# Optimization experiments

Hardware: AMD Instinct MI355X
Metric: run time of the kernel (lower is better)

The kernel has to match this reference:

```python
import jax, jax.numpy as jnp
import numpy as np
from jax import lax

DN = ('NCHW', 'OIHW', 'NCHW')
NUM_CODES = 8192


def _conv(x, w, b):
    # Conv2d(k=4, s=2, p=1)
    y = lax.conv_general_dilated(x, w, (2, 2), ((1, 1), (1, 1)), dimension_numbers=DN)
    return y + b[None, :, None, None]


def _convT(x, w, b):
    # ConvTranspose2d(k=4, s=2, p=1) as lhs-dilated conv; kernel already in equivalent OIHW layout
    y = lax.conv_general_dilated(x, w, (1, 1), ((2, 2), (2, 2)), lhs_dilation=(2, 2), dimension_numbers=DN)
    return y + b[None, :, None, None]


def _aff(x, s, b):
    # eval-mode BatchNorm folded to per-channel affine
    return x * s[None, :, None, None] + b[None, :, None, None]


def _forward(x, ew1, eb1, bn1s, bn1b, ew2, eb2, bn2s, bn2b, ew3, eb3, bn3s, bn3b, ew4, eb4, embed, cluster_size, dw1, db1, dbn1s, dbn1b, dw2, db2, dbn2s, dbn2b, dw3, db3, dbn3s, dbn3b, dw4, db4):
    sg = lax.stop_gradient
    embed = sg(embed)          # codebook is a torch buffer -> no grad
    cluster_size = sg(cluster_size)
    relu = jax.nn.relu
    # ---- Encoder: 4 stride-2 convs ----
    h = relu(_aff(_conv(x, ew1, eb1), bn1s, bn1b))
    h = relu(_aff(_conv(h, ew2, eb2), bn2s, bn2b))
    h = relu(_aff(_conv(h, ew3, eb3), bn3s, bn3b))
    z = _conv(h, ew4, eb4)                       # [B, D, G, G]
    zt = jnp.transpose(z, (0, 2, 3, 1))          # [B, G, G, D]
    D = zt.shape[-1]
    flat = zt.reshape(-1, D)                     # [N, D]
    N = flat.shape[0]
    # ---- VQ: pairwise squared distance + argmin codebook lookup ----
    dist = (flat * flat).sum(1, keepdims=True) - 2.0 * (flat @ embed.T) + (embed * embed).sum(1)[None, :]
    soft = jax.nn.softmax(-dist, axis=-1)        # temperature = 1.0
    codes = jnp.argmin(dist, axis=1)             # [N]
    zq = embed[codes]                            # [N, D]
    commitment_loss = jnp.mean((flat - sg(zq)) ** 2)
    codebook_loss = jnp.mean((zq - sg(flat)) ** 2)
    avg_soft = soft.mean(0)
    usage_entropy = -(avg_soft * jnp.log(avg_soft + 1e-10)).sum()
    diversity_loss = -usage_entropy / float(np.log(NUM_CODES))
    zq_st = flat + sg(zq - flat)                 # straight-through estimator
    zq_grid = jnp.transpose(zq_st.reshape(zt.shape), (0, 3, 1, 2))  # [B, D, G, G]
    # ---- Decoder: 4 stride-2 transposed convs ----
    h = relu(_aff(_convT(zq_grid, dw1, db1), dbn1s, dbn1b))
    h = relu(_aff(_convT(h, dw2, db2), dbn2s, dbn2b))
    h = relu(_aff(_convT(h, dw3, db3), dbn3s, dbn3b))
    recon = jax.nn.sigmoid(_convT(h, dw4, db4))
    recon_loss = jnp.mean((recon - x) ** 2)
    # ---- usage stats (no-grad in torch) ----
    hard_avg = jnp.zeros(NUM_CODES, flat.dtype).at[codes].add(1.0) / N
    perplexity = jnp.exp(-(hard_avg * jnp.log(hard_avg + 1e-10)).sum())
    active_codes = (cluster_size > 1).sum()
    codes_grid = codes.reshape(zt.shape[:-1])
    return (recon, recon_loss, codes_grid, zq_grid, commitment_loss, codebook_loss, diversity_loss, usage_entropy, perplexity, active_codes)


def setup_inputs() -> dict:
    keys = iter(jax.random.split(jax.random.key(0), 64))
    def randn(shape, s=1.0):
        return jax.random.normal(next(keys), shape, jnp.float32) * s
    def randu(shape):
        return jax.random.uniform(next(keys), shape, dtype=jnp.float32)
    B, H = 32, 256
    return {
        'x': randu((B, 1, H, H)),
        'ew1': randn((64, 1, 4, 4), 0.25), 'eb1': randn((64,), 0.1),
        'bn1s': randu((64,)), 'bn1b': randn((64,), 0.1),
        'ew2': randn((64, 64, 4, 4), 0.03), 'eb2': randn((64,), 0.1),
        'bn2s': randu((64,)), 'bn2b': randn((64,), 0.1),
        'ew3': randn((128, 64, 4, 4), 0.03), 'eb3': randn((128,), 0.1),
        'bn3s': randu((128,)), 'bn3b': randn((128,), 0.1),
        'ew4': randn((64, 128, 4, 4), 0.02), 'eb4': randn((64,), 0.1),
        'embed': randn((8192, 64), 0.5),
        'cluster_size': jnp.ones((8192,), jnp.float32),
        'dw1': randn((128, 64, 4, 4), 0.03), 'db1': randn((128,), 0.1),
        'dbn1s': randu((128,)), 'dbn1b': randn((128,), 0.1),
        'dw2': randn((64, 128, 4, 4), 0.02), 'db2': randn((64,), 0.1),
        'dbn2s': randu((64,)), 'dbn2b': randn((64,), 0.1),
        'dw3': randn((64, 64, 4, 4), 0.03), 'db3': randn((64,), 0.1),
        'dbn3s': randu((64,)), 'dbn3b': randn((64,), 0.1),
        'dw4': randn((1, 64, 4, 4), 0.03), 'db4': randn((1,), 0.1),
    }


def reference(x, ew1, eb1, bn1s, bn1b, ew2, eb2, bn2s, bn2b, ew3, eb3, bn3s, bn3b, ew4, eb4, embed, cluster_size, dw1, db1, dbn1s, dbn1b, dw2, db2, dbn2s, dbn2b, dw3, db3, dbn3s, dbn3b, dw4, db4):
    return _forward(x, ew1, eb1, bn1s, bn1b, ew2, eb2, bn2s, bn2b, ew3, eb3, bn3s, bn3b, ew4, eb4, embed, cluster_size, dw1, db1, dbn1s, dbn1b, dw2, db2, dbn2s, dbn2b, dw3, db3, dbn3s, dbn3b, dw4, db4)
```

## Files before the change

kernel.cpp:

```cpp
#include <hip/hip_runtime.h>
#include <cstdint>
#include <cstddef>


#define DEVI __device__ __forceinline__

typedef short  short8 __attribute__((ext_vector_type(8)));
typedef __bf16 bf16x8 __attribute__((ext_vector_type(8)));
typedef float  f32x16 __attribute__((ext_vector_type(16)));

DEVI f32x16 MFMA(bf16x8 a, bf16x8 b, f32x16 c){
  return __builtin_amdgcn_mfma_f32_32x32x16_bf16(a, b, c, 0, 0, 0);
}

DEVI ushort f2bf(float f){
  unsigned u = __float_as_uint(f);
  unsigned r = (u + 0x7FFFu + ((u >> 16) & 1u)) >> 16;
  return (ushort)r;
}
DEVI float bf2f(ushort h){ return __uint_as_float(((unsigned)h) << 16); }

union U8 { short8 s; bf16x8 b; };
DEVI bf16x8 ldg8u(const ushort* p){
  U8 u; u.s = *(const short8*)p; return u.b;
}

DEVI float wred64(float v){
  #pragma unroll
  for (int off=32; off>0; off>>=1) v += __shfl_down(v, off, 64);
  return v;
}

#define O_RECON     0
#define O_RLOSS     2097152
#define O_CODES     2097153
#define O_ZQ        2105345
#define O_COMMIT    2629633
#define O_CB        2629634
#define O_DIV       2629635
#define O_UE        2629636
#define O_PERP      2629637
#define O_ACT       2629638

#define WS_R1       0ull
#define A3H_OFF     0ull
#define A3M_OFF     8912896ull
#define A3L_OFF     17825792ull
#define PP_OFF      33554432ull
#define MT_OFF      37748736ull
#define PARTA_OFF   41943040ull
#define A2H_OFF     134217728ull
#define A2M_OFF     151519232ull
#define A2L_OFF     168820736ull
#define EH_OFF      134217728ull
#define EM_OFF      135266304ull
#define EL_OFF      136314880ull
#define FH_OFF      137363456ull
#define FM_OFF      138412032ull
#define FL_OFF      139460608ull
#define D2H_OFF     134217728ull
#define D2L_OFF     151519232ull
#define D1H_OFF     168820736ull
#define D1L_OFF     177733632ull
#define WS_FLAT     186646528ull
#define WS_ZQP      188743680ull
#define WS_WT       191102976ull
#define WT_E2       (WS_WT)
#define WT_E3       (WT_E2 + 393216ull)
#define WT_E4       (WT_E3 + 786432ull)
#define WT_D1       (WT_E4 + 786432ull)
#define WT_D2       (WT_D1 + 524288ull)
#define WT_D3       (WT_D2 + 524288ull)
#define WS_W4       (WT_D3 + 262144ull)
#define WS_STATS    (WS_W4 + 4096ull)
#define ST_RMP      (WS_STATS)
#define ST_CNT      (ST_RMP + 65536ull)
#define ST_AVGS     (ST_CNT + 32768ull)
#define ST_ROWZI    (ST_AVGS + 32768ull)
#define ST_CODESQ   (ST_ROWZI + 32768ull)
#define ST_LOSS     (ST_CODESQ + 32768ull)

__global__ __launch_bounds__(256) void k_init(unsigned int* __restrict__ cnt,
                                              unsigned long long* __restrict__ rmp,
                                              float* __restrict__ loss)
{
  int i = blockIdx.x*256 + threadIdx.x;
  if (i < 8192){ cnt[i]=0u; rmp[i]=0xFFFFFFFFFFFFFFFFull; }
  if (i < 8) loss[i]=0.f;
}

__global__ __launch_bounds__(256) void k_wsplit(
    const float* __restrict__ src, ushort* __restrict__ dh,
    ushort* __restrict__ dm, ushort* __restrict__ dl,
    int OC, int CIN, int isT, int three)
{
  int i = blockIdx.x*256 + threadIdx.x;
  if (i >= 16*OC*CIN) return;
  int cin = i % CIN; int t = i / CIN; int oc = t % OC; int tap = t / OC;
  int st;
  if (isT){
    int pq = tap>>2, ab = tap&3;
    int p = pq>>1, q = pq&1, a = ab>>1, b = ab&1;
    st = (p + 2*a)*4 + (q + 2*b);
  } else st = tap;
  float v = src[((size_t)oc*CIN + cin)*16 + st];
  ushort h = f2bf(v); float r = v - bf2f(h);
  if (three){
    ushort m = f2bf(r); float r2 = r - bf2f(m);
    dm[i] = m; dl[i] = f2bf(r2);
  } else {
    dl[i] = f2bf(r);
  }
  dh[i] = h;
}

__global__ __launch_bounds__(256) void k_w4prep(const float* __restrict__ dw4,
                                                float* __restrict__ w4)
{
  int i = blockIdx.x*256 + threadIdx.x;
  if (i >= 1024) return;
  int c = i & 63; int t16 = i >> 6;
  int pq = t16 >> 2, ab = t16 & 3;
  int p = pq>>1, q = pq&1, a = ab>>1, b = ab&1;
  w4[i] = dw4[(size_t)c*16 + (p+2*a)*4 + (q+2*b)];
}

__global__ __launch_bounds__(256) void k_esplit(
    const float* __restrict__ src, ushort* __restrict__ dh,
    ushort* __restrict__ dm, ushort* __restrict__ dl)
{
  int i = blockIdx.x*256 + threadIdx.x;
  float v = src[i];
  ushort h = f2bf(v); float r1 = v - bf2f(h);
  ushort m = f2bf(r1); float r2 = r1 - bf2f(m);
  dh[i] = h; dm[i] = m; dl[i] = f2bf(r2);
}

__global__ __launch_bounds__(256) void k_zpad3(unsigned* __restrict__ b0,
                                               unsigned* __restrict__ b1,
                                               unsigned* __restrict__ b2,
                                               int rows, int Wp, int cwords)
{
  int i = blockIdx.x*256 + threadIdx.x;
  int total = rows*2*cwords;
  if (i >= total) return;
  int pos = i / cwords, cw = i % cwords;
  int row = pos >> 1, side = pos & 1;
  size_t w = ((size_t)row*Wp + (side ? (Wp-1) : 0))*cwords + cw;
  b0[w] = 0u;
  if (b1) b1[w] = 0u;
  if (b2) b2[w] = 0u;
}

__global__ __launch_bounds__(256) void enc_conv1(
    const float* __restrict__ x, const float* __restrict__ w,
    const float* __restrict__ cb_, const float* __restrict__ bns,
    const float* __restrict__ bnb, float* __restrict__ out)
{
  __shared__ __align__(16) float sIn[34][36];
  __shared__ __align__(16) float sW[64][16];
  int b = blockIdx.x;
  int t = b & 63, n = b >> 6;
  int ty = t >> 3, tx = t & 7;
  int oy0 = ty*16, ox0 = tx*16;
  int iy0 = 2*oy0 - 1, ix0 = 2*ox0 - 1;
  int tid = threadIdx.x;
  int spg = tid & 31, og = tid >> 5;
  int sy = spg >> 1, x0 = (spg & 1)*8;

  if (tid < 64){
    const float* wp = w + tid*16;
    *(float4*)&sW[tid][0]  = *(const float4*)(wp);
    *(float4*)&sW[tid][4]  = *(const float4*)(wp+4);
    *(float4*)&sW[tid][8]  = *(const float4*)(wp+8);
    *(float4*)&sW[tid][12] = *(const float4*)(wp+12);
  }
  for (int e = tid; e < 34*34; e += 256){
    int rr = e/34, cc = e%34;
    int iy = iy0+rr, ix = ix0+cc;
    float v = 0.f;
    if ((unsigned)iy < 256u && (unsigned)ix < 256u)
      v = x[(size_t)n*65536 + iy*256 + ix];
    sIn[rr][cc] = v;
  }
  __syncthreads();

  float acc[8][8];
  #pragma unroll
  for (int j=0;j<8;j++)
    #pragma unroll
    for (int xi=0;xi<8;xi++) acc[j][xi]=0.f;

  #pragma unroll
  for (int ky=0; ky<4; ky++){
    int riy = 2*sy + ky;
    float seg[20];
    #pragma unroll
    for (int i=0;i<5;i++){
      float4 v = *(const float4*)&sIn[riy][2*x0 + 4*i];
      seg[4*i+0]=v.x; seg[4*i+1]=v.y; seg[4*i+2]=v.z; seg[4*i+3]=v.w;
    }
    #pragma unroll
    for (int j=0;j<8;j++){
      float4 w4v = *(const float4*)&sW[og*8+j][ky*4];
      #pragma unroll
      for (int xi=0; xi<8; xi++){
        acc[j][xi] = fmaf(seg[2*xi+0], w4v.x,
                     fmaf(seg[2*xi+1], w4v.y,
                     fmaf(seg[2*xi+2], w4v.z,
                     fmaf(seg[2*xi+3], w4v.w, acc[j][xi]))));
      }
    }
  }

  float sc[8], sh[8];
  #pragma unroll
  for (int j=0;j<8;j++){
    int oc = og*8+j;
    sc[j] = bns[oc];
    sh[j] = fmaf(cb_[oc], sc[j], bnb[oc]);
  }
  int oy = oy0 + sy;
  #pragma unroll
  for (int xi=0; xi<8; xi++){
    int oxg = ox0 + x0 + xi;
    float* op = out + (((size_t)n*128 + oy)*128 + oxg)*64 + og*8;
    float4 q0, q1;
    q0.x = fmaxf(fmaf(acc[0][xi], sc[0], sh[0]), 0.f);
    q0.y = fmaxf(fmaf(acc[1][xi], sc[1], sh[1]), 0.f);
    q0.z = fmaxf(fmaf(acc[2][xi], sc[2], sh[2]), 0.f);
    q0.w = fmaxf(fmaf(acc[3][xi], sc[3], sh[3]), 0.f);
    q1.x = fmaxf(fmaf(acc[4][xi], sc[4], sh[4]), 0.f);
    q1.y = fmaxf(fmaf(acc[5][xi], sc[5], sh[5]), 0.f);
    q1.z = fmaxf(fmaf(acc[6][xi], sc[6], sh[6]), 0.f);
    q1.w = fmaxf(fmaf(acc[7][xi], sc[7], sh[7]), 0.f);
    *(float4*)op     = q0;
    *(float4*)(op+4) = q1;
  }
}

template<int CIN, int OC, int OUTW, int OUTH, int INW, int INH, bool XPAD,
         int INMODE, int OUTMODE>
__global__ __launch_bounds__(256) void enc_conv(
    const float* __restrict__ in,
    const ushort* __restrict__ aH, const ushort* __restrict__ aM,
    const ushort* __restrict__ aL,
    const ushort* __restrict__ wtH, const ushort* __restrict__ wtM,
    const ushort* __restrict__ wtL,
    const float* __restrict__ cb_, const float* __restrict__ bns,
    const float* __restrict__ bnb,
    float* __restrict__ outF,
    ushort* __restrict__ oH, ushort* __restrict__ oM, ushort* __restrict__ oL,
    int nOcg)
{
  constexpr int INWP  = (INMODE==1) ? (INW+2) : (XPAD ? (INW+2) : INW);
  constexpr int WP    = INW + 2;
  constexpr int NROWS = 64 / OUTW;
  constexpr int AELEM = NROWS * WP * CIN;
  constexpr int BCIN  = (CIN > 64) ? 64 : CIN;
  constexpr int BELEM = 64 * BCIN;
  constexpr int SCRSZ = (3*BELEM*2 > 64*68*4) ? 3*BELEM*2 : 64*68*4;

  __shared__ __align__(16) ushort sAh[AELEM], sAm[AELEM], sAl[AELEM];
  __shared__ __align__(16) char sScr[SCRSZ];
  ushort* sBh = (ushort*)sScr;
  ushort* sBm = sBh + BELEM;
  ushort* sBl = sBm + BELEM;
  float*  sC  = (float*)sScr;

  int b = blockIdx.x;
  int ocg = b % nOcg; b /= nOcg;
  int yb  = b % (OUTH/NROWS); b /= (OUTH/NROWS);
  int n = b;
  int oy0 = yb * NROWS, oc0 = ocg * 64;

  int tid = threadIdx.x;
  int l = tid & 63, wave = tid >> 6;
  int wm = wave >> 1, wn = wave & 1;
  int r = l & 31, kp = l >> 5;
  int idx = wm*32 + r;
  int oy_off = idx / OUTW, ox = idx % OUTW;

  f32x16 acc;
  #pragma unroll
  for (int i=0;i<16;i++) acc[i] = 0.f;

  const size_t nbase = (size_t)n * INH * INWP * CIN;

  for (int ky = 0; ky < 4; ky++){
    __syncthreads();
    for (int c = tid; c < AELEM/8; c += 256){
      int j  = c / (WP*CIN/8);
      int rm = c % (WP*CIN/8);
      int lx = rm / (CIN/8);
      int c8 = (rm % (CIN/8)) * 8;
      int iy = 2*(oy0 + j) - 1 + ky;
      bool ok = (unsigned)iy < (unsigned)INH;
      unsigned off = (unsigned)(((j*WP + lx)*CIN + c8)*2) ^ ((((unsigned)lx>>1)&7u)<<4);
      if constexpr (INMODE == 0){
        int gx = XPAD ? lx : (lx - 1);
        if (!XPAD) ok = ok && ((unsigned)gx < (unsigned)INW);
        float4 v0 = {0,0,0,0}, v1 = {0,0,0,0};
        if (ok){
          const float* s = in + nbase + ((size_t)iy*INWP + gx)*CIN + c8;
          v0 = *(const float4*)s; v1 = *(const float4*)(s+4);
        }
        float vv[8] = {v0.x,v0.y,v0.z,v0.w,v1.x,v1.y,v1.z,v1.w};
        short8 hh, mm, ll;
        #pragma unroll
        for (int e=0;e<8;e++){
          ushort h = f2bf(vv[e]); float r1 = vv[e] - bf2f(h);
          ushort m = f2bf(r1);    float r2 = r1 - bf2f(m);
          hh[e] = (short)h; mm[e] = (short)m; ll[e] = (short)f2bf(r2);
        }
        *(short8*)((char*)sAh + off) = hh;
        *(short8*)((char*)sAm + off) = mm;
        *(short8*)((char*)sAl + off) = ll;
      } else {
        short8 vh = {0,0,0,0,0,0,0,0}, vm = vh, vl = vh;
        if (ok){
          size_t s = nbase + ((size_t)iy*INWP + lx)*CIN + c8;
          vh = *(const short8*)(aH + s);
          vm = *(const short8*)(aM + s);
          vl = *(const short8*)(aL + s);
        }
        *(short8*)((char*)sAh + off) = vh;
        *(short8*)((char*)sAm + off) = vm;
        *(short8*)((char*)sAl + off) = vl;
      }
    }
    for (int kx = 0; kx < 4; kx++){
      int tap = ky*4 + kx;
      for (int ch = 0; ch < CIN; ch += BCIN){
        __syncthreads();
        for (int c = tid; c < BELEM/8; c += 256){
          int oc = c / (BCIN/8);
          int c8 = (c % (BCIN/8)) * 8;
          size_t s = ((size_t)tap*OC + oc0 + oc)*CIN + ch + c8;
          unsigned off = (unsigned)((oc*BCIN + c8)*2) ^ (((unsigned)oc&7u)<<4);
          *(short8*)((char*)sBh + off) = *(const short8*)(wtH + s);
          *(short8*)((char*)sBm + off) = *(const short8*)(wtM + s);
          *(short8*)((char*)sBl + off) = *(const short8*)(wtL + s);
        }
        __syncthreads();
        int lx = 2*ox + kx;
        unsigned asw  = ((((unsigned)lx>>1)&7u)<<4);
        unsigned alin = (unsigned)(((oy_off*WP + lx)*CIN)*2);
        int ocl = wn*32 + r;
        unsigned bsw  = (((unsigned)ocl&7u)<<4);
        unsigned blin = (unsigned)((ocl*BCIN)*2);
        #pragma unroll
        for (int ct = 0; ct < BCIN/16; ct++){
          unsigned kbA = (unsigned)((ch + ct*16 + kp*8)*2);
          unsigned kbB = (unsigned)((ct*16 + kp*8)*2);
          unsigned ao = (alin + kbA) ^ asw;
          unsigned bo = (blin + kbB) ^ bsw;
          bf16x8 ah = *(const bf16x8*)((char*)sAh + ao);
          bf16x8 am = *(const bf16x8*)((char*)sAm + ao);
          bf16x8 al = *(const bf16x8*)((char*)sAl + ao);
          bf16x8 bh = *(const bf16x8*)((char*)sBh + bo);
          bf16x8 bm = *(const bf16x8*)((char*)sBm + bo);
          bf16x8 bl = *(const bf16x8*)((char*)sBl + bo);
          acc = MFMA(ah, bh, acc);
          acc = MFMA(ah, bm, acc);
          acc = MFMA(am, bh, acc);
          acc = MFMA(ah, bl, acc);
          acc = MFMA(am, bm, acc);
          acc = MFMA(al, bh, acc);
        }
      }
    }
  }
  __syncthreads();
  #pragma unroll
  for (int q = 0; q < 16; q++){
    int rowt = (q&3) + 8*(q>>2) + 4*kp;
    sC[(wm*32 + rowt)*68 + wn*32 + r] = acc[q];
  }
  __syncthreads();
  {
    int m = tid >> 2, qq = tid & 3;
    int oc = oc0 + qq*16;
    int oyg = oy0 + m / OUTW;
    int oxg = m % OUTW;
    if constexpr (OUTMODE == 1){
      size_t row = (size_t)n*256 + oyg*16 + oxg;
      float* op = outF + row*64 + qq*16;
      size_t pb = row*64 + qq*16;
      short8 hv[2], mv[2], lv[2];
      #pragma unroll
      for (int i=0;i<16;i++){
        float v = sC[m*68 + qq*16 + i] + cb_[oc+i];
        op[i] = v;
        ushort h = f2bf(v); float r1 = v - bf2f(h);
        ushort mm = f2bf(r1); float r2 = r1 - bf2f(mm);
        hv[i>>3][i&7]=(short)h; mv[i>>3][i&7]=(short)mm; lv[i>>3][i&7]=(short)f2bf(r2);
      }
      *(short8*)(oH + pb) = hv[0]; *(short8*)(oH + pb + 8) = hv[1];
      *(short8*)(oM + pb) = mv[0]; *(short8*)(oM + pb + 8) = mv[1];
      *(short8*)(oL + pb) = lv[0]; *(short8*)(oL + pb + 8) = lv[1];
    } else {
      size_t pbase = (((size_t)n*OUTH + oyg)*(OUTW+2) + oxg + 1)*OC + oc;
      short8 hv[2], mv[2], lv[2];
      #pragma unroll
      for (int i=0;i<16;i++){
        float s1 = bns[oc+i];
        float s2 = fmaf(cb_[oc+i], s1, bnb[oc+i]);
        float v = fmaxf(fmaf(sC[m*68 + qq*16 + i], s1, s2), 0.f);
        ushort h = f2bf(v); float r1 = v - bf2f(h);
        ushort mm = f2bf(r1); float r2 = r1 - bf2f(mm);
        hv[i>>3][i&7]=(short)h; mv[i>>3][i&7]=(short)mm; lv[i>>3][i&7]=(short)f2bf(r2);
      }
      *(short8*)(oH + pbase)   = hv[0]; *(short8*)(oH + pbase+8) = hv[1];
      *(short8*)(oM + pbase)   = mv[0]; *(short8*)(oM + pbase+8) = mv[1];
      *(short8*)(oL + pbase)   = lv[0]; *(short8*)(oL + pbase+8) = lv[1];
    }
  }
}

__global__ __launch_bounds__(256) void k_codesq(const float* __restrict__ embed,
                                                float* __restrict__ codesq)
{
  int j = blockIdx.x*4 + (threadIdx.x>>6);
  int c = threadIdx.x & 63;
  float e = embed[(size_t)j*64 + c];
  float s = wred64(e*e);
  if (c==0) codesq[j] = s;
}

DEVI float rmp_minval(unsigned long long v){
  unsigned skey = (unsigned)(v >> 32);
  unsigned u = (skey & 0x80000000u) ? (skey ^ 0x80000000u) : ~skey;
  return __uint_as_float(u);
}

__global__ __launch_bounds__(256) void vq_min(
    const ushort* __restrict__ fH, const ushort* __restrict__ fM,
    const ushort* __restrict__ fL,
    const ushort* __restrict__ eH, const ushort* __restrict__ eM,
    const ushort* __restrict__ eL,
    const float* __restrict__ codesq,
    unsigned long long* __restrict__ rmp,
    float* __restrict__ Pp, float* __restrict__ Mt)
{
  __shared__ __align__(16) ushort sAh[128*64], sAm[128*64], sAl[128*64];
  int cb = blockIdx.x & 63, rb = blockIdx.x >> 6;
  int row0 = rb*128, c0 = cb*128;
  int tid = threadIdx.x, l = tid&63, wave = tid>>6;
  int wm = wave>>1, wn = wave&1, r = l&31, kp = l>>5;

  for (int c = tid; c < 1024; c += 256){
    int rr = c >> 3, c8 = (c & 7)*8;
    size_t s = (size_t)(row0+rr)*64 + c8;
    unsigned off = (unsigned)((rr*64 + c8)*2) ^ (((unsigned)rr&7u)<<4);
    *(short8*)((char*)sAh + off) = *(const short8*)(fH + s);
    *(short8*)((char*)sAm + off) = *(const short8*)(fM + s);
    *(short8*)((char*)sAl + off) = *(const short8*)(fL + s);
  }
  __syncthreads();

  f32x16 acc[2][2];
  #pragma unroll
  for (int mt=0;mt<2;mt++)
    #pragma unroll
    for (int nt=0;nt<2;nt++)
      #pragma unroll
      for (int i=0;i<16;i++) acc[mt][nt][i]=0.f;

  #pragma unroll
  for (int ks=0; ks<4; ks++){
    unsigned kb = (unsigned)((ks*16 + kp*8)*2);
    int ko = ks*16 + kp*8;
    bf16x8 Ah[2],Am[2],Al[2],Bh[2],Bm[2],Bl[2];
    #pragma unroll
    for (int mt=0;mt<2;mt++){
      int rowi = wm*64 + mt*32 + r;
      unsigned o = ((unsigned)(rowi*128) + kb) ^ (((unsigned)rowi&7u)<<4);
      Ah[mt] = *(const bf16x8*)((char*)sAh + o);
      Am[mt] = *(const bf16x8*)((char*)sAm + o);
      Al[mt] = *(const bf16x8*)((char*)sAl + o);
    }
    #pragma unroll
    for (int nt=0;nt<2;nt++){
      int coli = c0 + wn*64 + nt*32 + r;
      size_t bo = (size_t)coli*64 + ko;
      Bh[nt] = ldg8u(eH + bo);
      Bm[nt] = ldg8u(eM + bo);
      Bl[nt] = ldg8u(eL + bo);
    }
    #pragma unroll
    for (int mt=0;mt<2;mt++)
      #pragma unroll
      for (int nt=0;nt<2;nt++){
        acc[mt][nt] = MFMA(Ah[mt], Bh[nt], acc[mt][nt]);
        acc[mt][nt] = MFMA(Ah[mt], Bm[nt], acc[mt][nt]);
        acc[mt][nt] = MFMA(Am[mt], Bh[nt], acc[mt][nt]);
        acc[mt][nt] = MFMA(Ah[mt], Bl[nt], acc[mt][nt]);
        acc[mt][nt] = MFMA(Am[mt], Bm[nt], acc[mt][nt]);
        acc[mt][nt] = MFMA(Al[mt], Bh[nt], acc[mt][nt]);
      }
  }

  float cq[2];
  cq[0] = codesq[c0 + wn*64 + r];
  cq[1] = codesq[c0 + wn*64 + 32 + r];
  #pragma unroll
  for (int mt=0; mt<2; mt++){
    #pragma unroll
    for (int q=0; q<16; q++){
      int rowt = (q&3) + 8*(q>>2) + 4*kp;
      int grow = row0 + wm*64 + mt*32 + rowt;
      float dv[2];
      unsigned long long kmin = 0xFFFFFFFFFFFFFFFFull;
      #pragma unroll
      for (int nt=0; nt<2; nt++){
        int col = c0 + wn*64 + nt*32 + r;
        float d = cq[nt] - 2.f*acc[mt][nt][q];
        dv[nt] = d;
        unsigned u = __float_as_uint(d);
        unsigned sgn = (unsigned)((int)u >> 31);
        unsigned skey = u ^ (sgn | 0x80000000u);
        unsigned long long key = (((unsigned long long)skey)<<32) | (unsigned)col;
        if (key < kmin) kmin = key;
      }
      #pragma unroll
      for (int off2=16; off2>0; off2>>=1){
        unsigned long long o2 = __shfl_xor(kmin, off2, 64);
        if (o2 < kmin) kmin = o2;
      }
      float mloc = rmp_minval(kmin);
      float p = __expf(mloc - dv[0]) + __expf(mloc - dv[1]);
      #pragma unroll
      for (int off2=16; off2>0; off2>>=1) p += __shfl_xor(p, off2, 64);
      if (r == 0){
        atomicMin(&rmp[grow], kmin);
        size_t pidx = (size_t)grow*128 + (size_t)cb*2 + wn;
        Pp[pidx] = p;
        Mt[pidx] = mloc;
      }
    }
  }
}

__global__ __launch_bounds__(256) void k_rowz2(
    const unsigned long long* __restrict__ rmp,
    const float* __restrict__ Pp, const float* __restrict__ Mt,
    float* __restrict__ rowzi)
{
  int row = blockIdx.x*256 + threadIdx.x;
  float mg = rmp_minval(rmp[row]);
  const float* pp = Pp + (size_t)row*128;
  const float* mt = Mt + (size_t)row*128;
  float z = 0.f;
  for (int t = 0; t < 128; t++)
    z = fmaf(__expf(mg - mt[t]), pp[t], z);
  rowzi[row] = 1.f / z;
}

__global__ __launch_bounds__(256) void vq_avg(
    const ushort* __restrict__ fH, const ushort* __restrict__ fM,
    const ushort* __restrict__ fL,
    const ushort* __restrict__ eH, const ushort* __restrict__ eM,
    const ushort* __restrict__ eL,
    const float* __restrict__ codesq,
    const unsigned long long* __restrict__ rmp,
    const float* __restrict__ rowzi,
    float* __restrict__ partA)
{
  __shared__ __align__(16) ushort sAh[128*64], sAm[128*64], sAl[128*64];
  __shared__ float colbuf[128];
  int cb = blockIdx.x & 63, rb = blockIdx.x >> 6;
  int row0 = rb*128, c0 = cb*128;
  int tid = threadIdx.x, l = tid&63, wave = tid>>6;
  int wm = wave>>1, wn = wave&1, r = l&31, kp = l>>5;

  if (tid < 128) colbuf[tid] = 0.f;

  for (int c = tid; c < 1024; c += 256){
    int rr = c >> 3, c8 = (c & 7)*8;
    size_t s = (size_t)(row0+rr)*64 + c8;
    unsigned off = (unsigned)((rr*64 + c8)*2) ^ (((unsigned)rr&7u)<<4);
    *(short8*)((char*)sAh + off) = *(const short8*)(fH + s);
    *(short8*)((char*)sAm + off) = *(const short8*)(fM + s);
    *(short8*)((char*)sAl + off) = *(const short8*)(fL + s);
  }
  __syncthreads();

  f32x16 acc[2][2];
  #pragma unroll
  for (int mt=0;mt<2;mt++)
    #pragma unroll
    for (int nt=0;nt<2;nt++)
      #pragma unroll
      for (int i=0;i<16;i++) acc[mt][nt][i]=0.f;

  #pragma unroll
  for (int ks=0; ks<4; ks++){
    unsigned kb = (unsigned)((ks*16 + kp*8)*2);
    int ko = ks*16 + kp*8;
    bf16x8 Ah[2],Am[2],Al[2],Bh[2],Bm[2],Bl[2];
    #pragma unroll
    for (int mt=0;mt<2;mt++){
      int rowi = wm*64 + mt*32 + r;
      unsigned o = ((unsigned)(rowi*128) + kb) ^ (((unsigned)rowi&7u)<<4);
      Ah[mt] = *(const bf16x8*)((char*)sAh + o);
      Am[mt] = *(const bf16x8*)((char*)sAm + o);
      Al[mt] = *(const bf16x8*)((char*)sAl + o);
    }
    #pragma unroll
    for (int nt=0;nt<2;nt++){
      int coli = c0 + wn*64 + nt*32 + r;
      size_t bo = (size_t)coli*64 + ko;
      Bh[nt] = ldg8u(eH + bo);
      Bm[nt] = ldg8u(eM + bo);
      Bl[nt] = ldg8u(eL + bo);
    }
    #pragma unroll
    for (int mt=0;mt<2;mt++)
      #pragma unroll
      for (int nt=0;nt<2;nt++){
        acc[mt][nt] = MFMA(Ah[mt], Bh[nt], acc[mt][nt]);
        acc[mt][nt] = MFMA(Ah[mt], Bm[nt], acc[mt][nt]);
        acc[mt][nt] = MFMA(Am[mt], Bh[nt], acc[mt][nt]);
        acc[mt][nt] = MFMA(Ah[mt], Bl[nt], acc[mt][nt]);
        acc[mt][nt] = MFMA(Am[mt], Bm[nt], acc[mt][nt]);
        acc[mt][nt] = MFMA(Al[mt], Bh[nt], acc[mt][nt]);
      }
  }

  float cq[2];
  cq[0] = codesq[c0 + wn*64 + r];
  cq[1] = codesq[c0 + wn*64 + 32 + r];
  float colacc[2] = {0.f, 0.f};
  #pragma unroll
  for (int mt=0; mt<2; mt++){
    #pragma unroll
    for (int q=0; q<16; q++){
      int rowt = (q&3) + 8*(q>>2) + 4*kp;
      int grow = row0 + wm*64 + mt*32 + rowt;
      float mi = rmp_minval(rmp[grow]);
      float zi = rowzi[grow];
      #pragma unroll
      for (int nt=0; nt<2; nt++){
        float d = cq[nt] - 2.f*acc[mt][nt][q];
        colacc[nt] = fmaf(__expf(mi - d), zi, colacc[nt]);
      }
    }
  }
  #pragma unroll
  for (int nt=0; nt<2; nt++){
    float o = __shfl_xor(colacc[nt], 32, 64);
    colacc[nt] += o;
    if (l < 32) atomicAdd(&colbuf[wn*64 + nt*32 + r], colacc[nt]);
  }
  __syncthreads();
  if (tid < 128)
    partA[(size_t)rb*8192 + c0 + tid] = colbuf[tid];
}

__global__ __launch_bounds__(256) void k_avgred(const float* __restrict__ partA,
                                                float* __restrict__ avgs)
{
  int j = blockIdx.x*256 + threadIdx.x;
  float s = 0.f;
  for (int rb = 0; rb < 64; rb++)
    s += partA[(size_t)rb*8192 + j];
  avgs[j] = s;
}

__global__ __launch_bounds__(256) void vq_post(
    const float* __restrict__ flat, const float* __restrict__ embed,
    const unsigned long long* __restrict__ rmp,
    float* __restrict__ out_codes, float* __restrict__ out_zq,
    ushort* __restrict__ zqPh, ushort* __restrict__ zqPl,
    float* __restrict__ loss, unsigned int* __restrict__ cnt)
{
  int r = blockIdx.x*4 + (threadIdx.x>>6);
  int c = threadIdx.x & 63;
  unsigned j = (unsigned)(rmp[r] & 0xFFFFFFFFull);
  float e = embed[(size_t)j*64 + c];
  float f = flat[(size_t)r*64 + c];
  int n = r>>8, rem = r&255, gy = rem>>4, gx = rem&15;
  out_zq[(((size_t)n*64 + c)*16 + gy)*16 + gx] = e;
  ushort h = f2bf(e);
  size_t pz = (((size_t)n*16 + gy)*18 + gx + 1)*64 + c;
  zqPh[pz] = h; zqPl[pz] = f2bf(e - bf2f(h));
  float d = f - e;
  float s2 = wred64(d*d);
  if (c==0){
    out_codes[r] = (float)j;
    atomicAdd(cnt + j, 1u);
    atomicAdd(loss + 1, s2);
  }
}

template<int CIN, int OC, int SW, int SH, bool OUTPAD, int OMODE, int NPAR>
__global__ __launch_bounds__(256) void dec_convT_m(
    const ushort* __restrict__ inH, const ushort* __restrict__ inL,
    const ushort* __restrict__ wtH, const ushort* __restrict__ wtL,
    const float* __restrict__ db, const float* __restrict__ bns,
    const float* __restrict__ bnb,
    ushort* __restrict__ oH, ushort* __restrict__ oL, int nOcg)
{
  constexpr int TR    = 64 / SW;
  constexpr int NRA   = TR + ((NPAR==4) ? 2 : 1);
  constexpr int WPin  = SW + 2;
  constexpr int AELEM = NRA * WPin * CIN;
  constexpr int OUTH  = 2*SH;
  constexpr int OW    = OUTPAD ? (2*SW+2) : (2*SW);

  __shared__ __align__(16) ushort sAh[AELEM], sAl[AELEM];
  __shared__ __align__(16) float sC[64*68];

  int b = blockIdx.x;
  int p_blk = 0;
  if (NPAR == 2){ p_blk = b & 1; b >>= 1; }
  int ocg = b % nOcg; b /= nOcg;
  int tb = b % (SH/TR); b /= (SH/TR);
  int n = b;
  int t0 = tb * TR, oc0 = ocg * 64;
  const int ROWBASE = (NPAR==4) ? -1 : (p_blk - 1);

  int tid = threadIdx.x, l = tid&63, wave = tid>>6;
  int wm = wave>>1, wn = wave&1;
  int r = l&31, kp = l>>5;
  int idx = wm*32 + r;
  int t_off = idx / SW, s = idx % SW;
  int ocl = oc0 + wn*32 + r;

  for (int c = tid; c < AELEM/8; c += 256){
    int j  = c / (WPin*CIN/8);
    int rm = c % (WPin*CIN/8);
    int lx = rm / (CIN/8);
    int c8 = (rm % (CIN/8)) * 8;
    int giy = t0 + ROWBASE + j;
    bool ok = (unsigned)giy < (unsigned)SH;
    short8 vh = {0,0,0,0,0,0,0,0}, vl = {0,0,0,0,0,0,0,0};
    if (ok){
      size_t sidx = (((size_t)n*SH + giy)*WPin + lx)*CIN + c8;
      vh = *(const short8*)(inH + sidx);
      vl = *(const short8*)(inL + sidx);
    }
    unsigned off = (unsigned)(((j*WPin + lx)*CIN + c8)*2) ^ (((unsigned)lx&7u)<<4);
    *(short8*)((char*)sAh + off) = vh;
    *(short8*)((char*)sAl + off) = vl;
  }
  __syncthreads();

  for (int pr = 0; pr < NPAR; pr++){
    int p2 = (NPAR==4) ? (pr>>1) : p_blk;
    int q2 = (NPAR==4) ? (pr&1)  : pr;
    int par = p2*2 + q2;

    f32x16 acc;
    #pragma unroll
    for (int i=0;i<16;i++) acc[i]=0.f;

    for (int ab = 0; ab < 4; ab++){
      int a = ab>>1, bb = ab&1;
      int rs = t_off + ((NPAR==4) ? (p2 + a) : a);
      int lx = s + q2 + bb;
      unsigned asw  = (((unsigned)lx&7u)<<4);
      unsigned alin = (unsigned)(((rs*WPin + lx)*CIN)*2);
      size_t brow = ((size_t)(par*4 + ab)*OC + ocl)*CIN;
      #pragma unroll
      for (int ct = 0; ct < CIN/16; ct++){
        int ko = ct*16 + kp*8;
        unsigned ao = (alin + (unsigned)(ko*2)) ^ asw;
        bf16x8 ah = *(const bf16x8*)((char*)sAh + ao);
        bf16x8 al = *(const bf16x8*)((char*)sAl + ao);
        bf16x8 bh = ldg8u(wtH + brow + ko);
        bf16x8 bl = ldg8u(wtL + brow + ko);
        acc = MFMA(ah, bh, acc);
        acc = MFMA(ah, bl, acc);
        acc = MFMA(al, bh, acc);
      }
    }

    __syncthreads();
    #pragma unroll
    for (int qre = 0; qre < 16; qre++){
      int rowt = (qre&3) + 8*(qre>>2) + 4*kp;
      sC[(wm*32 + rowt)*68 + wn*32 + r] = acc[qre];
    }
    __syncthreads();
    {
      int m = tid >> 2, qq = tid & 3;
      int oc = oc0 + qq*16;
      int y  = 2*(t0 + m/SW) + p2;
      int xs = m % SW;
      int xp = OUTPAD ? (2*xs + q2 + 1) : (2*xs + q2);
      size_t base = (((size_t)n*OUTH + y)*OW + xp)*OC + oc;
      if constexpr (OMODE == 2){
        short8 h0[2];
        #pragma unroll
        for (int i=0;i<16;i++){
          float s1 = bns[oc+i];
          float s2 = fmaf(db[oc+i], s1, bnb[oc+i]);
          float v = fmaxf(fmaf(sC[m*68 + qq*16 + i], s1, s2), 0.f);
          h0[i>>3][i&7] = (short)f2bf(v);
        }
        *(short8*)(oH + base)     = h0[0];
        *(short8*)(oH + base + 8) = h0[1];
      } else {
        short8 h0[2], l0[2];
        #pragma unroll
        for (int i=0;i<16;i++){
          float s1 = bns[oc+i];
          float s2 = fmaf(db[oc+i], s1, bnb[oc+i]);
          float v = fmaxf(fmaf(sC[m*68 + qq*16 + i], s1, s2), 0.f);
          ushort h = f2bf(v);
          ushort lo = f2bf(v - bf2f(h));
          h0[i>>3][i&7]=(short)h; l0[i>>3][i&7]=(short)lo;
        }
        *(short8*)(oH + base)     = h0[0];
        *(short8*)(oH + base + 8) = h0[1];
        *(short8*)(oL + base)     = l0[0];
        *(short8*)(oL + base + 8) = l0[1];
      }
    }
  }
}

__global__ __launch_bounds__(256) void dec_convT4(
    const ushort* __restrict__ d3, const float* __restrict__ w4,
    const float* __restrict__ db4, const float* __restrict__ xref,
    float* __restrict__ recon, float* __restrict__ loss)
{
  __shared__ __align__(16) float sT[10*10*68];
  __shared__ __align__(16) float sWt[16*64];
  __shared__ float red[4];
  int b = blockIdx.x;
  int t = b & 255, n = b >> 8;
  int ty = t >> 4, tx = t & 15;
  int y0 = ty*16, x0 = tx*16;
  int r0 = y0/2 - 1, c0 = x0/2 - 1;
  int tid = threadIdx.x;

  *(float4*)&sWt[tid*4] = *(const float4*)(w4 + tid*4);

  const ushort* base = d3 + (size_t)n*128*128*64;
  for (int e = tid; e < 800; e += 256){
    int rr = e/80; int rem = e%80; int cc = rem/8; int c8 = (rem%8)*8;
    int gr = r0+rr, gc = c0+cc;
    short8 v = {0,0,0,0,0,0,0,0};
    if ((unsigned)gr<128u && (unsigned)gc<128u)
      v = *(const short8*)(base + ((size_t)gr*128+gc)*64 + c8);
    float* dst = &sT[(rr*10+cc)*68 + c8];
    float4 f0, f1;
    f0.x = bf2f((ushort)v[0]); f0.y = bf2f((ushort)v[1]);
    f0.z = bf2f((ushort)v[2]); f0.w = bf2f((ushort)v[3]);
    f1.x = bf2f((ushort)v[4]); f1.y = bf2f((ushort)v[5]);
    f1.z = bf2f((ushort)v[6]); f1.w = bf2f((ushort)v[7]);
    *(float4*)dst     = f0;
    *(float4*)(dst+4) = f1;
  }
  __syncthreads();

  int sy = tid>>4, sx = tid&15;
  int p = sy&1, q = sx&1;
  int lr0 = (sy>>1)+p, lc0 = (sx>>1)+q;
  int par = p*2+q;
  float4 a4 = {0,0,0,0};
  #pragma unroll
  for (int a=0;a<2;a++){
    #pragma unroll
    for (int bb=0;bb<2;bb++){
      const float* ip = &sT[((lr0+a)*10 + lc0+bb)*68];
      const float* wp = &sWt[(par*4+a*2+bb)*64];
      #pragma unroll
      for (int c=0;c<64;c+=4){
        float4 v  = *(const float4*)(ip+c);
        float4 wv = *(const float4*)(wp+c);
        a4.x = fmaf(v.x, wv.x, a4.x);
        a4.y = fmaf(v.y, wv.y, a4.y);
        a4.z = fmaf(v.z, wv.z, a4.z);
        a4.w = fmaf(v.w, wv.w, a4.w);
      }
    }
  }
  float acc = (a4.x + a4.y) + (a4.z + a4.w);
  float v = acc + db4[0];
  float rcn = 1.f/(1.f + __expf(-v));
  int y = y0+sy, x = x0+sx;
  size_t oi = (size_t)n*65536 + (size_t)y*256 + x;
  recon[oi] = rcn;
  float d = rcn - xref[oi];
  float s2 = wred64(d*d);
  if ((tid & 63)==0) red[tid>>6] = s2;
  __syncthreads();
  if (tid==0) atomicAdd(loss + 0, red[0]+red[1]+red[2]+red[3]);
}

__global__ __launch_bounds__(256) void k_final(
    const float* __restrict__ avgs, const unsigned int* __restrict__ cnt,
    const float* __restrict__ cluster, const float* __restrict__ loss,
    float* __restrict__ dout)
{
  __shared__ float red[3][4];
  int tid = threadIdx.x;
  float e1=0.f, e2=0.f, ac=0.f;
  for (int j=tid; j<8192; j+=256){
    float a = avgs[j] * (1.f/8192.f);
    e1 += a * __logf(a + 1e-10f);
    float h = (float)cnt[j] * (1.f/8192.f);
    e2 += h * __logf(h + 1e-10f);
    ac += (cluster[j] > 1.f) ? 1.f : 0.f;
  }
  e1 = wred64(e1); e2 = wred64(e2); ac = wred64(ac);
  int wv = tid >> 6;
  if ((tid & 63)==0){ red[0][wv]=e1; red[1][wv]=e2; red[2][wv]=ac; }
  __syncthreads();
  if (tid==0){
    float s1 = red[0][0]+red[0][1]+red[0][2]+red[0][3];
    float s2 = red[1][0]+red[1][1]+red[1][2]+red[1][3];
    float s3 = red[2][0]+red[2][1]+red[2][2]+red[2][3];
    float ue = -s1;
    dout[O_RLOSS]  = loss[0] * (1.f/2097152.f);
    float cc = loss[1] * (1.f/524288.f);
    dout[O_COMMIT] = cc;
    dout[O_CB]     = cc;
    dout[O_DIV]    = -ue / 9.010913347279288f;
    dout[O_UE]     = ue;
    dout[O_PERP]   = __expf(-s2);
    dout[O_ACT]    = s3;
  }
}

extern "C" void kernel_launch(void* const* d_in, const int* in_sizes, int n_in,
                              void* d_out, int out_size, void* d_ws, size_t ws_size,
                              hipStream_t stream)
{
  (void)in_sizes; (void)n_in; (void)out_size; (void)ws_size;
  const float* x     = (const float*)d_in[0];
  const float* ew1   = (const float*)d_in[1];
  const float* eb1   = (const float*)d_in[2];
  const float* bn1s  = (const float*)d_in[3];
  const float* bn1b  = (const float*)d_in[4];
  const float* ew2   = (const float*)d_in[5];
  const float* eb2   = (const float*)d_in[6];
  const float* bn2s  = (const float*)d_in[7];
  const float* bn2b  = (const float*)d_in[8];
  const float* ew3   = (const float*)d_in[9];
  const float* eb3   = (const float*)d_in[10];
  const float* bn3s  = (const float*)d_in[11];
  const float* bn3b  = (const float*)d_in[12];
  const float* ew4   = (const float*)d_in[13];
  const float* eb4   = (const float*)d_in[14];
  const float* embed = (const float*)d_in[15];
  const float* clsz  = (const float*)d_in[16];
  const float* dw1   = (const float*)d_in[17];
  const float* db1   = (const float*)d_in[18];
  const float* dbn1s = (const float*)d_in[19];
  const float* dbn1b = (const float*)d_in[20];
  const float* dw2   = (const float*)d_in[21];
  const float* db2   = (const float*)d_in[22];
  const float* dbn2s = (const float*)d_in[23];
  const float* dbn2b = (const float*)d_in[24];
  const float* dw3   = (const float*)d_in[25];
  const float* db3   = (const float*)d_in[26];
  const float* dbn3s = (const float*)d_in[27];
  const float* dbn3b = (const float*)d_in[28];
  const float* dw4   = (const float*)d_in[29];
  const float* db4   = (const float*)d_in[30];

  float* out = (float*)d_out;
  uint8_t* wsb = (uint8_t*)d_ws;

  float*  A1   = (float*)(wsb + WS_R1);
  ushort* D3b  = (ushort*)(wsb + WS_R1);
  ushort* A3h  = (ushort*)(wsb + A3H_OFF);
  ushort* A3m  = (ushort*)(wsb + A3M_OFF);
  ushort* A3l  = (ushort*)(wsb + A3L_OFF);
  float*  Pp   = (float*)(wsb + PP_OFF);
  float*  Mt   = (float*)(wsb + MT_OFF);
  float*  partA= (float*)(wsb + PARTA_OFF);
  ushort* A2h  = (ushort*)(wsb + A2H_OFF);
  ushort* A2m  = (ushort*)(wsb + A2M_OFF);
  ushort* A2l  = (ushort*)(wsb + A2L_OFF);
  ushort* eH   = (ushort*)(wsb + EH_OFF);
  ushort* eM   = (ushort*)(wsb + EM_OFF);
  ushort* eL   = (ushort*)(wsb + EL_OFF);
  ushort* fH   = (ushort*)(wsb + FH_OFF);
  ushort* fM   = (ushort*)(wsb + FM_OFF);
  ushort* fL   = (ushort*)(wsb + FL_OFF);
  ushort* D1h  = (ushort*)(wsb + D1H_OFF);
  ushort* D1l  = (ushort*)(wsb + D1L_OFF);
  ushort* D2h  = (ushort*)(wsb + D2H_OFF);
  ushort* D2l  = (ushort*)(wsb + D2L_OFF);
  float*  flat = (float*)(wsb + WS_FLAT);
  ushort* zqPh = (ushort*)(wsb + WS_ZQP);
  ushort* zqPl = (ushort*)(wsb + WS_ZQP + 1179648ull);

  ushort* wE2h = (ushort*)(wsb + WT_E2);
  ushort* wE2m = wE2h + 65536;  ushort* wE2l = wE2m + 65536;
  ushort* wE3h = (ushort*)(wsb + WT_E3);
  ushort* wE3m = wE3h + 131072; ushort* wE3l = wE3m + 131072;
  ushort* wE4h = (ushort*)(wsb + WT_E4);
  ushort* wE4m = wE4h + 131072; ushort* wE4l = wE4m + 131072;
  ushort* wD1h = (ushort*)(wsb + WT_D1);
  ushort* wD1l = wD1h + 131072;
  ushort* wD2h = (ushort*)(wsb + WT_D2);
  ushort* wD2l = wD2h + 131072;
  ushort* wD3h = (ushort*)(wsb + WT_D3);
  ushort* wD3l = wD3h + 65536;
  float*  w4   = (float*)(wsb + WS_W4);

  unsigned long long* rmp = (unsigned long long*)(wsb + ST_RMP);
  unsigned int* cnt = (unsigned int*)(wsb + ST_CNT);
  float* avgs   = (float*)(wsb + ST_AVGS);
  float* rowzi  = (float*)(wsb + ST_ROWZI);
  float* codesq = (float*)(wsb + ST_CODESQ);
  float* loss   = (float*)(wsb + ST_LOSS);

  dim3 B(256);

  k_init<<<32, B, 0, stream>>>(cnt, rmp, loss);

  k_wsplit<<<256, B, 0, stream>>>(ew2, wE2h, wE2m, wE2l, 64, 64, 0, 1);
  k_wsplit<<<512, B, 0, stream>>>(ew3, wE3h, wE3m, wE3l, 128, 64, 0, 1);
  k_wsplit<<<512, B, 0, stream>>>(ew4, wE4h, wE4m, wE4l, 64, 128, 0, 1);
  k_wsplit<<<512, B, 0, stream>>>(dw1, wD1h, nullptr, wD1l, 128, 64, 1, 0);
  k_wsplit<<<512, B, 0, stream>>>(dw2, wD2h, nullptr, wD2l, 64, 128, 1, 0);
  k_wsplit<<<256, B, 0, stream>>>(dw3, wD3h, nullptr, wD3l, 64, 64, 1, 0);
  k_w4prep<<<4, B, 0, stream>>>(dw4, w4);

  k_zpad3<<<512, B, 0, stream>>>((unsigned*)A2h, (unsigned*)A2m, (unsigned*)A2l,
                                 32*64, 66, 32);
  k_zpad3<<<128, B, 0, stream>>>((unsigned*)zqPh, (unsigned*)zqPl, nullptr,
                                 32*16, 18, 32);

  enc_conv1<<<2048, B, 0, stream>>>(x, ew1, eb1, bn1s, bn1b, A1);
  enc_conv<64,64,64,64,128,128,false,0,0><<<2048, B, 0, stream>>>(
      A1, nullptr, nullptr, nullptr, wE2h, wE2m, wE2l, eb2, bn2s, bn2b,
      nullptr, A2h, A2m, A2l, 1);
  k_zpad3<<<512, B, 0, stream>>>((unsigned*)A3h, (unsigned*)A3m, (unsigned*)A3l,
                                 32*32, 34, 64);
  enc_conv<64,128,32,32,64,64,true,1,0><<<1024, B, 0, stream>>>(
      nullptr, A2h, A2m, A2l, wE3h, wE3m, wE3l, eb3, bn3s, bn3b,
      nullptr, A3h, A3m, A3l, 2);
  k_esplit<<<2048, B, 0, stream>>>(embed, eH, eM, eL);
  enc_conv<128,64,16,16,32,32,true,1,1><<<128, B, 0, stream>>>(
      nullptr, A3h, A3m, A3l, wE4h, wE4m, wE4l, eb4, eb4, eb4,
      flat, fH, fM, fL, 1);

  k_codesq<<<2048, B, 0, stream>>>(embed, codesq);

  vq_min<<<4096, B, 0, stream>>>(fH, fM, fL, eH, eM, eL, codesq, rmp, Pp, Mt);
  k_rowz2<<<32, B, 0, stream>>>(rmp, Pp, Mt, rowzi);
  vq_avg<<<4096, B, 0, stream>>>(fH, fM, fL, eH, eM, eL, codesq, rmp, rowzi, partA);
  k_avgred<<<32, B, 0, stream>>>(partA, avgs);

  vq_post<<<2048, B, 0, stream>>>(flat, embed, rmp, out + O_CODES, out + O_ZQ,
                                  zqPh, zqPl, loss, cnt);

  k_zpad3<<<512, B, 0, stream>>>((unsigned*)D1h, (unsigned*)D1l, nullptr, 32*32, 34, 64);
  k_zpad3<<<512, B, 0, stream>>>((unsigned*)D2h, (unsigned*)D2l, nullptr, 32*64, 66, 32);

  dec_convT_m<64,128,16,16,true,0,4><<<256, B, 0, stream>>>(
      zqPh, zqPl, wD1h, wD1l, db1, dbn1s, dbn1b, D1h, D1l, 2);
  dec_convT_m<128,64,32,32,true,0,2><<<1024, B, 0, stream>>>(
      D1h, D1l, wD2h, wD2l, db2, dbn2s, dbn2b, D2h, D2l, 1);
  dec_convT_m<64,64,64,64,false,2,4><<<2048, B, 0, stream>>>(
      D2h, D2l, wD3h, wD3l, db3, dbn3s, dbn3b, D3b, nullptr, 1);
  dec_convT4<<<8192, B, 0, stream>>>(D3b, w4, db4, x, out + O_RECON, loss);

  k_final<<<1, B, 0, stream>>>(avgs, cnt, clsz, loss, out);
}
```

Measured before the change: 1.088 ms.

## Transpose vq_min tile so codes are MFMA rows, reducing min in-register

The vq_min GEMM now puts codebook rows in the LDS-staged A operand and flat vectors in the streamed B operand. Each lane then holds 32 code distances for one flat row, so the per-row argmin and softmax partial sum are done in registers with a single cross-half shuffle. This replaces 32 per-row five-step shuffle reductions and many small atomics and stores. k_rowz2 also writes the per-row min as a float, so vq_avg reads it directly instead of decoding the packed rmp key. Workspace grows by one array, and the Pp/Mt column index changes from wn to wm.

```diff
diff --git a/kernel.cpp b/kernel.cpp
--- a/kernel.cpp
+++ b/kernel.cpp
@@ -79,6 +79,7 @@
 #define ST_ROWZI    (ST_AVGS + 32768ull)
 #define ST_CODESQ   (ST_ROWZI + 32768ull)
 #define ST_LOSS     (ST_CODESQ + 32768ull)
+#define ST_ROWM     (ST_LOSS + 32768ull)
 
 __global__ __launch_bounds__(256) void k_init(unsigned int* __restrict__ cnt,
                                               unsigned long long* __restrict__ rmp,
@@ -444,18 +445,18 @@
     float* __restrict__ Pp, float* __restrict__ Mt)
 {
   __shared__ __align__(16) ushort sAh[128*64], sAm[128*64], sAl[128*64];
-  int cb = blockIdx.x & 63, rb = blockIdx.x >> 6;
-  int row0 = rb*128, c0 = cb*128;
+  int cblk = blockIdx.x & 63, fblk = blockIdx.x >> 6;
+  int code0 = cblk*128, f0 = fblk*128;
   int tid = threadIdx.x, l = tid&63, wave = tid>>6;
   int wm = wave>>1, wn = wave&1, r = l&31, kp = l>>5;
 
   for (int c = tid; c < 1024; c += 256){
     int rr = c >> 3, c8 = (c & 7)*8;
-    size_t s = (size_t)(row0+rr)*64 + c8;
+    size_t s = (size_t)(code0+rr)*64 + c8;
     unsigned off = (unsigned)((rr*64 + c8)*2) ^ (((unsigned)rr&7u)<<4);
-    *(short8*)((char*)sAh + off) = *(const short8*)(fH + s);
-    *(short8*)((char*)sAm + off) = *(const short8*)(fM + s);
-    *(short8*)((char*)sAl + off) = *(const short8*)(fL + s);
+    *(short8*)((char*)sAh + off) = *(const short8*)(eH + s);
+    *(short8*)((char*)sAm + off) = *(const short8*)(eM + s);
+    *(short8*)((char*)sAl + off) = *(const short8*)(eL + s);
   }
   __syncthreads();
 
@@ -482,11 +483,11 @@
     }
     #pragma unroll
     for (int nt=0;nt<2;nt++){
-      int coli = c0 + wn*64 + nt*32 + r;
+      int coli = f0 + wn*64 + nt*32 + r;
       size_t bo = (size_t)coli*64 + ko;
-      Bh[nt] = ldg8u(eH + bo);
-      Bm[nt] = ldg8u(eM + bo);
-      Bl[nt] = ldg8u(eL + bo);
+      Bh[nt] = ldg8u(fH + bo);
+      Bm[nt] = ldg8u(fM + bo);
+      Bl[nt] = ldg8u(fL + bo);
     }
     #pragma unroll
     for (int mt=0;mt<2;mt++)
@@ -501,43 +502,49 @@
       }
   }
 
-  float cq[2];
-  cq[0] = codesq[c0 + wn*64 + r];
-  cq[1] = codesq[c0 + wn*64 + 32 + r];
-  #pragma unroll
-  for (int mt=0; mt<2; mt++){
-    #pragma unroll
-    for (int q=0; q<16; q++){
-      int rowt = (q&3) + 8*(q>>2) + 4*kp;
-      int grow = row0 + wm*64 + mt*32 + rowt;
-      float dv[2];
-      unsigned long long kmin = 0xFFFFFFFFFFFFFFFFull;
-      #pragma unroll
-      for (int nt=0; nt<2; nt++){
-        int col = c0 + wn*64 + nt*32 + r;
-        float d = cq[nt] - 2.f*acc[mt][nt][q];
-        dv[nt] = d;
+  float cqv[2][16];
+  #pragma unroll
+  for (int mt=0; mt<2; mt++)
+    #pragma unroll
+    for (int g=0; g<4; g++){
+      float4 cv = *(const float4*)(codesq + code0 + wm*64 + mt*32 + 8*g + 4*kp);
+      cqv[mt][4*g+0]=cv.x; cqv[mt][4*g+1]=cv.y;
+      cqv[mt][4*g+2]=cv.z; cqv[mt][4*g+3]=cv.w;
+    }
+
+  #pragma unroll
+  for (int nt=0; nt<2; nt++){
+    int col = f0 + wn*64 + nt*32 + r;
+    unsigned long long kmin = 0xFFFFFFFFFFFFFFFFull;
+    #pragma unroll
+    for (int mt=0; mt<2; mt++)
+      #pragma unroll
+      for (int q=0; q<16; q++){
+        float d = cqv[mt][q] - 2.f*acc[mt][nt][q];
+        int code = code0 + wm*64 + mt*32 + (q&3) + 8*(q>>2) + 4*kp;
         unsigned u = __float_as_uint(d);
         unsigned sgn = (unsigned)((int)u >> 31);
         unsigned skey = u ^ (sgn | 0x80000000u);
-        unsigned long long key = (((unsigned long long)skey)<<32) | (unsigned)col;
+        unsigned long long key = (((unsigned long long)skey)<<32) | (unsigned)code;
         if (key < kmin) kmin = key;
       }
-      #pragma unroll
-      for (int off2=16; off2>0; off2>>=1){
-        unsigned long long o2 = __shfl_xor(kmin, off2, 64);
-        if (o2 < kmin) kmin = o2;
-      }
-      float mloc = rmp_minval(kmin);
-      float p = __expf(mloc - dv[0]) + __expf(mloc - dv[1]);
-      #pragma unroll
-      for (int off2=16; off2>0; off2>>=1) p += __shfl_xor(p, off2, 64);
-      if (r == 0){
-        atomicMin(&rmp[grow], kmin);
-        size_t pidx = (size_t)grow*128 + (size_t)cb*2 + wn;
-        Pp[pidx] = p;
-        Mt[pidx] = mloc;
-      }
+    unsigned long long o2 = __shfl_xor(kmin, 32, 64);
+    if (o2 < kmin) kmin = o2;
+    float mloc = rmp_minval(kmin);
+    float p = 0.f;
+    #pragma unroll
+    for (int mt=0; mt<2; mt++)
+      #pragma unroll
+      for (int q=0; q<16; q++){
+        float d = cqv[mt][q] - 2.f*acc[mt][nt][q];
+        p += __expf(mloc - d);
+      }
+    p += __shfl_xor(p, 32, 64);
+    if (kp == 0){
+      atomicMin(&rmp[col], kmin);
+      size_t pidx = (size_t)col*128 + (size_t)cblk*2 + wm;
+      Pp[pidx] = p;
+      Mt[pidx] = mloc;
     }
   }
 }
@@ -545,7 +552,7 @@
 __global__ __launch_bounds__(256) void k_rowz2(
     const unsigned long long* __restrict__ rmp,
     const float* __restrict__ Pp, const float* __restrict__ Mt,
-    float* __restrict__ rowzi)
+    float* __restrict__ rowzi, float* __restrict__ rowm)
 {
   int row = blockIdx.x*256 + threadIdx.x;
   float mg = rmp_minval(rmp[row]);
@@ -555,6 +562,7 @@
   for (int t = 0; t < 128; t++)
     z = fmaf(__expf(mg - mt[t]), pp[t], z);
   rowzi[row] = 1.f / z;
+  rowm[row] = mg;
 }
 
 __global__ __launch_bounds__(256) void vq_avg(
@@ -563,7 +571,7 @@
     const ushort* __restrict__ eH, const ushort* __restrict__ eM,
     const ushort* __restrict__ eL,
     const float* __restrict__ codesq,
-    const unsigned long long* __restrict__ rmp,
+    const float* __restrict__ rowm,
     const float* __restrict__ rowzi,
     float* __restrict__ partA)
 {
@@ -638,7 +646,7 @@
     for (int q=0; q<16; q++){
       int rowt = (q&3) + 8*(q>>2) + 4*kp;
       int grow = row0 + wm*64 + mt*32 + rowt;
-      float mi = rmp_minval(rmp[grow]);
+      float mi = rowm[grow];
       float zi = rowzi[grow];
       #pragma unroll
       for (int nt=0; nt<2; nt++){
@@ -1012,6 +1020,7 @@
   float* rowzi  = (float*)(wsb + ST_ROWZI);
   float* codesq = (float*)(wsb + ST_CODESQ);
   float* loss   = (float*)(wsb + ST_LOSS);
+  float* rowm   = (float*)(wsb + ST_ROWM);
 
   dim3 B(256);
 
@@ -1047,8 +1056,8 @@
   k_codesq<<<2048, B, 0, stream>>>(embed, codesq);
 
   vq_min<<<4096, B, 0, stream>>>(fH, fM, fL, eH, eM, eL, codesq, rmp, Pp, Mt);
-  k_rowz2<<<32, B, 0, stream>>>(rmp, Pp, Mt, rowzi);
-  vq_avg<<<4096, B, 0, stream>>>(fH, fM, fL, eH, eM, eL, codesq, rmp, rowzi, partA);
+  k_rowz2<<<32, B, 0, stream>>>(rmp, Pp, Mt, rowzi, rowm);
+  vq_avg<<<4096, B, 0, stream>>>(fH, fM, fL, eH, eM, eL, codesq, rowm, rowzi, partA);
   k_avgred<<<32, B, 0, stream>>>(partA, avgs);
 
   vq_post<<<2048, B, 0, stream>>>(flat, embed, rmp, out + O_CODES, out + O_ZQ,
```

Result: faster. 1.000 ms (-8.1%).
